# Kernel tuning notes

Hardware: AMD Instinct MI355X
Metric: run time of the kernel (lower is better)

Reference implementation:

```python
import jax, jax.numpy as jnp
import numpy as np

B, L, V, E_ENC, D_DEC, E_EMB = 256, 128, 4096, 1024, 1024, 512


def _lin(key, out_f, in_f, scale=0.02):
    k1, k2 = jax.random.split(key)
    return (jax.random.normal(k1, (out_f, in_f), jnp.float32) * scale,
            jax.random.normal(k2, (out_f,), jnp.float32) * scale)


def setup_inputs() -> dict:
    key = jax.random.key(0)
    ks = jax.random.split(key, 12)
    x = jax.random.normal(ks[0], (B, 1, V), jnp.float32)
    hidden = jax.random.normal(ks[1], (1, B, D_DEC), jnp.float32)
    enc_output = jax.random.normal(ks[2], (B, L, E_ENC), jnp.float32)
    W1_w, W1_b = _lin(ks[3], D_DEC, E_ENC)
    W2_w, W2_b = _lin(ks[4], D_DEC, D_DEC)
    V_w, V_b = _lin(ks[5], 1, D_DEC)
    out2emb_w, out2emb_b = _lin(ks[6], E_EMB, V)
    gru_wi, gru_bi = _lin(ks[7], 3 * D_DEC, E_EMB + E_ENC)
    gru_wh, gru_bh = _lin(ks[8], 3 * D_DEC, D_DEC)
    fc1_w, fc1_b = _lin(ks[9], E_EMB, D_DEC)
    fc2_w, fc2_b = _lin(ks[10], V, E_EMB)
    return dict(x=x, hidden=hidden, enc_output=enc_output,
                W1_w=W1_w, W1_b=W1_b, W2_w=W2_w, W2_b=W2_b, V_w=V_w, V_b=V_b,
                out2emb_w=out2emb_w, out2emb_b=out2emb_b,
                gru_wi=gru_wi, gru_wh=gru_wh, gru_bi=gru_bi, gru_bh=gru_bh,
                fc1_w=fc1_w, fc1_b=fc1_b, fc2_w=fc2_w, fc2_b=fc2_b)


def reference(x, hidden, enc_output, W1_w, W1_b, W2_w, W2_b, V_w, V_b,
              out2emb_w, out2emb_b, gru_wi, gru_wh, gru_bi, gru_bh,
              fc1_w, fc1_b, fc2_w, fc2_b):
    # --- Bahdanau additive attention ---
    h_t = hidden[-1][:, None, :]                                   # (B,1,dec)
    score = jnp.tanh(enc_output @ W1_w.T + W1_b + h_t @ W2_w.T + W2_b)  # (B,L,dec)
    attn = jax.nn.softmax(score @ V_w.T + V_b, axis=1)             # (B,L,1)
    context = jnp.sum(attn * enc_output, axis=1)                   # (B,enc)
    # --- embed previous output distribution ---
    x_emb = x @ out2emb_w.T + out2emb_b                            # (B,1,emb)
    rnn_in = jnp.concatenate([context[:, None, :], x_emb], -1)[:, 0, :]  # (B,emb+enc)
    # --- single GRU step (PyTorch gate layout r,z,n) ---
    h0 = hidden[0]
    gi = rnn_in @ gru_wi.T + gru_bi
    gh = h0 @ gru_wh.T + gru_bh
    ir, iz, inn = jnp.split(gi, 3, axis=-1)
    hr, hz, hn = jnp.split(gh, 3, axis=-1)
    r = jax.nn.sigmoid(ir + hr)
    z = jax.nn.sigmoid(iz + hz)
    n = jnp.tanh(inn + r * hn)
    h_new = (1.0 - z) * n + z * h0                                 # (B,dec)
    # --- output MLP ---
    out = jnp.tanh(h_new @ fc1_w.T + fc1_b) @ fc2_w.T + fc2_b      # (B,vocab)
    return out, h_new[None], attn
```

## Files before the change

### kernel.cpp

```cpp
#include <hip/hip_runtime.h>
#include <math.h>


#define B_   256
#define L_   128
#define V_   4096
#define ENC_ 1024
#define DEC_ 1024
#define EMB_ 512
#define MB_  1048576ull

typedef __bf16 bf16;
typedef __bf16 bf16x8 __attribute__((ext_vector_type(8)));
typedef __bf16 bf16x4 __attribute__((ext_vector_type(4)));
typedef float  f32x4  __attribute__((ext_vector_type(4)));

__device__ __forceinline__ float fast_tanh(float x) {
  float e = __builtin_amdgcn_exp2f(x * 2.88539008177792681472f);
  return 1.0f - 2.0f * __builtin_amdgcn_rcpf(e + 1.0f);
}
__device__ __forceinline__ float fast_sigmoid(float x) {
  return __builtin_amdgcn_rcpf(1.0f + __builtin_amdgcn_exp2f(-1.44269504088896f * x));
}

__device__ __forceinline__ void cp16(const void* g, void* l) {
  __builtin_amdgcn_global_load_lds(
      (const __attribute__((address_space(1))) void*)g,
      (__attribute__((address_space(3))) void*)l,
      16, 0, 0);
}

__device__ __forceinline__ bf16x8 ld8f(const float* f) {
  f32x4 a = *(const f32x4*)f;
  f32x4 b = *(const f32x4*)(f + 4);
  bf16x8 r;
  r[0] = (bf16)a[0]; r[1] = (bf16)a[1]; r[2] = (bf16)a[2]; r[3] = (bf16)a[3];
  r[4] = (bf16)b[0]; r[5] = (bf16)b[1]; r[6] = (bf16)b[2]; r[7] = (bf16)b[3];
  return r;
}


__device__ __forceinline__ void gemm64_f32(
    const float* __restrict__ A, const float* __restrict__ Brow,
    int strideA, int strideB, int kbeg, int kend, int row0,
    bf16* As, bf16* Bs, f32x4 acc[4])
{
  const int t   = threadIdx.x;
  const int lane = t & 63, w = t >> 6, q = lane >> 4, c16 = lane & 15;
  const int sr  = t >> 3, lb = t & 7;

  for (int k0 = kbeg; k0 < kend; k0 += 64) {
    bf16x8 va[2], vb[2];
#pragma unroll
    for (int ch = 0; ch < 2; ch++) {
      int r    = ch * 32 + sr;
      int gcol = k0 + ((lb ^ (r & 7)) << 3);
      va[ch] = ld8f(A    + (size_t)(row0 + r) * strideA + gcol);
      vb[ch] = ld8f(Brow + (size_t)r * strideB + gcol);
    }
#pragma unroll
    for (int ch = 0; ch < 2; ch++) {
      *(bf16x8*)&As[ch * 2048 + t * 8] = va[ch];
      *(bf16x8*)&Bs[ch * 2048 + t * 8] = vb[ch];
    }
    __syncthreads();
#pragma unroll
    for (int kkb = 0; kkb < 8; kkb += 4) {
      int rb = w * 16 + c16;
      bf16x8 bfr = *(const bf16x8*)&Bs[rb * 64 + (((kkb + q) ^ (rb & 7)) << 3)];
#pragma unroll
      for (int i = 0; i < 4; i++) {
        int ra = i * 16 + c16;
        bf16x8 af = *(const bf16x8*)&As[ra * 64 + (((kkb + q) ^ (ra & 7)) << 3)];
        acc[i] = __builtin_amdgcn_mfma_f32_16x16x32_bf16(af, bfr, acc[i], 0, 0, 0);
      }
    }
    __syncthreads();
  }
}

__global__ __launch_bounds__(256) void setup_k(
    const float* __restrict__ hidden, const float* __restrict__ W2,
    const float* __restrict__ wh, const float* __restrict__ W1_b,
    const float* __restrict__ W2_b, const float* __restrict__ gbh,
    const float* __restrict__ x, const float* __restrict__ o2e,
    const float* __restrict__ enc, const float* __restrict__ W1,
    const float* __restrict__ wi, const float* __restrict__ fc1w,
    const float* __restrict__ fc2w,
    bf16* __restrict__ enc_bf, bf16* __restrict__ W1_bf,
    bf16* __restrict__ wi_bf, bf16* __restrict__ fc1_bf,
    bf16* __restrict__ fc2_bf,
    bf16* __restrict__ u, bf16* __restrict__ gh, float* __restrict__ xe4)
{
  __shared__ __align__(16) bf16 As[64 * 64];
  __shared__ __align__(16) bf16 Bs[64 * 64];

  const int bid = blockIdx.x;
  const int t   = threadIdx.x;

  if (bid >= 384) {
    int i = bid - 384;
    const float* src; bf16* dst; int blk;
    if      (i < 8192) { src = enc;  dst = enc_bf; blk = i; }
    else if (i < 8448) { src = W1;   dst = W1_bf;  blk = i - 8192; }
    else if (i < 9600) { src = wi;   dst = wi_bf;  blk = i - 8448; }
    else if (i < 9728) { src = fc1w; dst = fc1_bf; blk = i - 9600; }
    else               { src = fc2w; dst = fc2_bf; blk = i - 9728; }
    const size_t base = (size_t)blk * 4096 + t * 16;
    const float* s = src + base;
    bf16* d = dst + base;
    *(bf16x8*)(d)     = ld8f(s);
    *(bf16x8*)(d + 8) = ld8f(s + 8);
    return;
  }

  const int lane = t & 63, w = t >> 6, q = lane >> 4, c16 = lane & 15;
  f32x4 acc[4] = {};

  if (bid < 256) {
    const int row0 = (bid >> 6) * 64;
    const int col0 = (bid & 63) * 64;
    const bool isU = (col0 < 1024);
    const float* Brow = isU ? (W2 + (size_t)col0 * 1024)
                            : (wh + (size_t)(col0 - 1024) * 1024);
    gemm64_f32(hidden, Brow, 1024, 1024, 0, 1024, row0, As, Bs, acc);

    const int gc = col0 + w * 16 + c16;
    float bias = isU ? (W1_b[gc] + W2_b[gc]) : gbh[gc - 1024];
#pragma unroll
    for (int i = 0; i < 4; i++) {
      int gr0 = row0 + i * 16 + q * 4;
#pragma unroll
      for (int r = 0; r < 4; r++) {
        float v = acc[i][r] + bias;
        if (isU) u[(size_t)(gr0 + r) * 1024 + gc] = (bf16)v;
        else     gh[(size_t)(gr0 + r) * 3072 + (gc - 1024)] = (bf16)v;
      }
    }
  } else {
    const int i3   = bid - 256;
    const int col0 = (i3 & 7) * 64;
    const int row0 = ((i3 >> 3) & 3) * 64;
    const int z    = i3 >> 5;
    gemm64_f32(x, o2e + (size_t)col0 * 4096, 4096, 4096,
               z * 1024, z * 1024 + 1024, row0, As, Bs, acc);

    const int gc = col0 + w * 16 + c16;
    float* out = xe4 + (size_t)z * 131072;
#pragma unroll
    for (int i = 0; i < 4; i++) {
      int gr0 = row0 + i * 16 + q * 4;
#pragma unroll
      for (int r = 0; r < 4; r++)
        out[(size_t)(gr0 + r) * 512 + gc] = acc[i][r];
    }
  }
}

__global__ __launch_bounds__(256) void score_f2(
    const bf16* __restrict__ A,
    const bf16* __restrict__ Bw,
    const bf16* __restrict__ u,
    const float* __restrict__ Vw,
    float* __restrict__ e_part)
{
  __shared__ __align__(16) bf16 As[128 * 64];
  __shared__ __align__(16) bf16 Bs[128 * 64];
  __shared__ float s_part[2][128];

  const int t    = threadIdx.x;
  const int lane = t & 63;
  const int w    = t >> 6;
  const int wm   = w >> 1;
  const int wn   = w & 1;
  const int q    = lane >> 4;
  const int c16  = lane & 15;
  const int sr   = t >> 3;
  const int lb   = t & 7;

  const int row0 = blockIdx.y * 128;
  const int b    = blockIdx.y;

  float rowsum[4][4] = {};

#pragma unroll 1
  for (int cbp = 0; cbp < 2; cbp++) {
    const int col0 = (blockIdx.x * 2 + cbp) * 128;
    f32x4 acc[4][4] = {};

    for (int k0 = 0; k0 < 1024; k0 += 64) {
#pragma unroll
      for (int ch = 0; ch < 4; ch++) {
        int r    = ch * 32 + sr;
        int gcol = k0 + ((lb ^ (r & 7)) << 3);
        cp16(A  + (size_t)(row0 + r) * 1024 + gcol, &As[ch * 2048 + t * 8]);
        cp16(Bw + (size_t)(col0 + r) * 1024 + gcol, &Bs[ch * 2048 + t * 8]);
      }
      __syncthreads();
#pragma unroll
      for (int kkb = 0; kkb < 8; kkb += 4) {
        bf16x8 af[4], bfr[4];
#pragma unroll
        for (int i = 0; i < 4; i++) {
          int ra = wm * 64 + i * 16 + c16;
          af[i] = *(const bf16x8*)&As[ra * 64 + (((kkb + q) ^ (ra & 7)) << 3)];
        }
#pragma unroll
        for (int j = 0; j < 4; j++) {
          int rb = wn * 64 + j * 16 + c16;
          bfr[j] = *(const bf16x8*)&Bs[rb * 64 + (((kkb + q) ^ (rb & 7)) << 3)];
        }
#pragma unroll
        for (int i = 0; i < 4; i++)
#pragma unroll
          for (int j = 0; j < 4; j++)
            acc[i][j] = __builtin_amdgcn_mfma_f32_16x16x32_bf16(af[i], bfr[j], acc[i][j], 0, 0, 0);
      }
      __syncthreads();
    }

#pragma unroll
    for (int i = 0; i < 4; i++) {
#pragma unroll
      for (int j = 0; j < 4; j++) {
        int gc   = col0 + wn * 64 + j * 16 + c16;
        float uc = (float)u[b * 1024 + gc];
        float vw = Vw[gc];
#pragma unroll
        for (int r = 0; r < 4; r++)
          rowsum[i][r] += fast_tanh(acc[i][j][r] + uc) * vw;
      }
    }
  }

#pragma unroll
  for (int i = 0; i < 4; i++) {
#pragma unroll
    for (int r = 0; r < 4; r++) {
      float v = rowsum[i][r];
      v += __shfl_xor(v, 1);
      v += __shfl_xor(v, 2);
      v += __shfl_xor(v, 4);
      v += __shfl_xor(v, 8);
      if (c16 == 0) s_part[wn][wm * 64 + i * 16 + q * 4 + r] = v;
    }
  }
  __syncthreads();
  if (t < 128)
    e_part[(size_t)blockIdx.x * 32768 + row0 + t] = s_part[0][t] + s_part[1][t];
}

__global__ __launch_bounds__(256) void softmax_f(
    const float* __restrict__ e_part,
    const bf16* __restrict__ enc,
    const float* __restrict__ xe4,
    const float* __restrict__ o2eb,
    float* __restrict__ attn_out,
    bf16* __restrict__ rnn_in)
{
  const int b = blockIdx.x;
  const int t = threadIdx.x;
  __shared__ float se[128];

  if (t < 128) {
    float s = 0.0f;
#pragma unroll
    for (int cb = 0; cb < 4; cb++) s += e_part[(size_t)cb * 32768 + b * 128 + t];
    se[t] = s;
  }
  __syncthreads();

  float m = -1e30f;
  for (int l = 0; l < 128; l++) m = fmaxf(m, se[l]);
  float sum = 0.0f;
  for (int l = 0; l < 128; l++) sum += expf(se[l] - m);
  float inv = 1.0f / sum;
  __syncthreads();
  if (t < 128) {
    float p = expf(se[t] - m) * inv;
    attn_out[b * 128 + t] = p;
    se[t] = p;
  }
  __syncthreads();

  float a0 = 0, a1 = 0, a2 = 0, a3 = 0;
  const bf16* ep = enc + (size_t)b * L_ * ENC_ + t * 4;
  for (int l = 0; l < 128; l++) {
    float p = se[l];
    bf16x4 v = *(const bf16x4*)(ep + (size_t)l * ENC_);
    a0 += p * (float)v[0]; a1 += p * (float)v[1];
    a2 += p * (float)v[2]; a3 += p * (float)v[3];
  }
  bf16x4 o;
  o[0] = (bf16)a0; o[1] = (bf16)a1; o[2] = (bf16)a2; o[3] = (bf16)a3;
  *(bf16x4*)(rnn_in + (size_t)b * 1536 + t * 4) = o;

#pragma unroll
  for (int jj = 0; jj < 2; jj++) {
    int j = jj * 256 + t;
    float v = o2eb[j];
#pragma unroll
    for (int z = 0; z < 4; z++) v += xe4[(size_t)z * 131072 + b * 512 + j];
    rnn_in[(size_t)b * 1536 + 1024 + j] = (bf16)v;
  }
}

template <int ACT, int OUTF32>
__global__ __launch_bounds__(256) void gemm_f(
    const bf16* __restrict__ A, const bf16* __restrict__ Bw,
    const float* __restrict__ bias1,
    void* __restrict__ C, int K, int out_ld)
{
  __shared__ __align__(16) bf16 As[64 * 64];
  __shared__ __align__(16) bf16 Bs[64 * 64];

  const int t    = threadIdx.x;
  const int lane = t & 63;
  const int w    = t >> 6;
  const int q    = lane >> 4;
  const int c16  = lane & 15;
  const int sr   = t >> 3;
  const int lb   = t & 7;
  const int row0 = blockIdx.y * 64;
  const int col0 = blockIdx.x * 64;

  f32x4 acc[4] = {};

  for (int k0 = 0; k0 < K; k0 += 64) {
#pragma unroll
    for (int ch = 0; ch < 2; ch++) {
      int r    = ch * 32 + sr;
      int gcol = k0 + ((lb ^ (r & 7)) << 3);
      cp16(A  + (size_t)(row0 + r) * K + gcol, &As[ch * 2048 + t * 8]);
      cp16(Bw + (size_t)(col0 + r) * K + gcol, &Bs[ch * 2048 + t * 8]);
    }
    __syncthreads();
#pragma unroll
    for (int kkb = 0; kkb < 8; kkb += 4) {
      int rb = w * 16 + c16;
      bf16x8 bfr = *(const bf16x8*)&Bs[rb * 64 + (((kkb + q) ^ (rb & 7)) << 3)];
#pragma unroll
      for (int i = 0; i < 4; i++) {
        int ra = i * 16 + c16;
        bf16x8 af = *(const bf16x8*)&As[ra * 64 + (((kkb + q) ^ (ra & 7)) << 3)];
        acc[i] = __builtin_amdgcn_mfma_f32_16x16x32_bf16(af, bfr, acc[i], 0, 0, 0);
      }
    }
    __syncthreads();
  }

  const int gc = col0 + w * 16 + c16;
  float bias = bias1[gc];
#pragma unroll
  for (int i = 0; i < 4; i++) {
    int gr0 = row0 + i * 16 + q * 4;
#pragma unroll
    for (int r = 0; r < 4; r++) {
      float v = acc[i][r] + bias;
      if (ACT == 1) v = fast_tanh(v);
      size_t off = (size_t)(gr0 + r) * out_ld + gc;
      if (OUTF32) ((float*)C)[off] = v;
      else        ((bf16*)C)[off] = (bf16)v;
    }
  }
}

__global__ __launch_bounds__(256) void gru_f(
    const bf16* __restrict__ gi, const bf16* __restrict__ gh,
    const float* __restrict__ h0,
    float* __restrict__ hnew_out, bf16* __restrict__ hnew_i)
{
  int idx = blockIdx.x * 256 + threadIdx.x;
  int b = idx >> 10, d = idx & 1023;
  const bf16* gib = gi + b * 3072;
  const bf16* ghb = gh + b * 3072;
  float ir = (float)gib[d], iz = (float)gib[1024 + d], in = (float)gib[2048 + d];
  float hr = (float)ghb[d], hz = (float)ghb[1024 + d], hn = (float)ghb[2048 + d];
  float r = fast_sigmoid(ir + hr);
  float z = fast_sigmoid(iz + hz);
  float n = fast_tanh(in + r * hn);
  float h = (1.0f - z) * n + z * h0[idx];
  hnew_out[idx] = h;
  hnew_i[idx]   = (bf16)h;
}

extern "C" void kernel_launch(void* const* d_in, const int* in_sizes, int n_in,
                              void* d_out, int out_size, void* d_ws, size_t ws_size,
                              hipStream_t stream) {
  const float* x      = (const float*)d_in[0];
  const float* hidden = (const float*)d_in[1];
  const float* enc    = (const float*)d_in[2];
  const float* W1_w   = (const float*)d_in[3];
  const float* W1_b   = (const float*)d_in[4];
  const float* W2_w   = (const float*)d_in[5];
  const float* W2_b   = (const float*)d_in[6];
  const float* V_w    = (const float*)d_in[7];
  const float* o2e_w  = (const float*)d_in[9];
  const float* o2e_b  = (const float*)d_in[10];
  const float* gru_wi = (const float*)d_in[11];
  const float* gru_wh = (const float*)d_in[12];
  const float* gru_bi = (const float*)d_in[13];
  const float* gru_bh = (const float*)d_in[14];
  const float* fc1_w  = (const float*)d_in[15];
  const float* fc1_b  = (const float*)d_in[16];
  const float* fc2_w  = (const float*)d_in[17];
  const float* fc2_b  = (const float*)d_in[18];

  float* out_main = (float*)d_out;
  float* out_h    = out_main + (size_t)B_ * V_;
  float* out_attn = out_h + (size_t)B_ * DEC_;

  char* ws = (char*)d_ws;
  bf16*  enc_bf  = (bf16*)(ws);
  bf16*  W1_bf   = (bf16*)(ws + 64 * MB_);
  bf16*  wi_bf   = (bf16*)(ws + 66 * MB_);
  bf16*  fc1_bf  = (bf16*)(ws + 75 * MB_);
  bf16*  fc2_bf  = (bf16*)(ws + 76 * MB_);
  bf16*  u_bf    = (bf16*)(ws + 80 * MB_);
  bf16*  gh_bf   = (bf16*)(ws + 80 * MB_ + 524288);
  float* e_part  = (float*)(ws + 82 * MB_);
  bf16*  gi_bf   = (bf16*)(ws + 82 * MB_ + 524288);
  bf16*  rnn_in  = (bf16*)(ws + 84 * MB_);
  bf16*  tbuf    = (bf16*)(ws + 84 * MB_ + 786432);
  bf16*  hnew_bf = (bf16*)(ws + 85 * MB_);
  float* xe4     = (float*)(ws + 85 * MB_ + 524288);

  setup_k<<<10624, 256, 0, stream>>>(
      hidden, W2_w, gru_wh, W1_b, W2_b, gru_bh, x, o2e_w,
      enc, W1_w, gru_wi, fc1_w, fc2_w,
      enc_bf, W1_bf, wi_bf, fc1_bf, fc2_bf, u_bf, gh_bf, xe4);

  score_f2<<<dim3(4, 256), 256, 0, stream>>>(enc_bf, W1_bf, u_bf, V_w, e_part);

  softmax_f<<<B_, 256, 0, stream>>>(e_part, enc_bf, xe4, o2e_b, out_attn, rnn_in);

  gemm_f<0, 0><<<dim3(48, 4), 256, 0, stream>>>(rnn_in, wi_bf, gru_bi, gi_bf, 1536, 3072);

  gru_f<<<(B_ * DEC_) / 256, 256, 0, stream>>>(gi_bf, gh_bf, hidden, out_h, hnew_bf);

  gemm_f<1, 0><<<dim3(8, 4), 256, 0, stream>>>(hnew_bf, fc1_bf, fc1_b, tbuf, 1024, 512);

  gemm_f<0, 1><<<dim3(64, 4), 256, 0, stream>>>(tbuf, fc2_bf, fc2_b, out_main, 512, 4096);
}
```

Baseline: 432.7 us.

## Rewrite attention score GEMM with 256x256 tiles and double-buffered LDS pipeline

The score kernel moves from 128x128 tiles with single-buffered LDS and a barrier-bound loop to 256x256 tiles on 512-thread blocks with two LDS stages. The next k-tile is prefetched while MFMAs run, and the blocks get a swizzled order for better L2 locality. The tanh and V-dot epilogue now runs once per tile instead of across two column passes, cutting global load traffic per FLOP. In exchange it uses much more LDS (128KB) and more accumulator registers per thread, which may limit occupancy.

```diff
diff --git a/kernel.cpp b/kernel.cpp
--- a/kernel.cpp
+++ b/kernel.cpp
@@ -157,97 +157,113 @@
   }
 }
 
-__global__ __launch_bounds__(256) void score_f2(
+__device__ __forceinline__ void stage_tile256(
+    const bf16* __restrict__ A, const bf16* __restrict__ Bw,
+    bf16* As, bf16* Bs, int row0, int col0, int k0, int t)
+{
+  const int sr = t >> 3, lb = t & 7;
+#pragma unroll
+  for (int ch = 0; ch < 4; ch++) {
+    int r    = ch * 64 + sr;
+    int gcol = k0 + ((lb ^ (r & 7)) << 3);
+    cp16(A  + (size_t)(row0 + r) * 1024 + gcol, &As[r * 64 + lb * 8]);
+    cp16(Bw + (size_t)(col0 + r) * 1024 + gcol, &Bs[r * 64 + lb * 8]);
+  }
+}
+
+__global__ __launch_bounds__(512, 2) void score_8p(
     const bf16* __restrict__ A,
     const bf16* __restrict__ Bw,
     const bf16* __restrict__ u,
     const float* __restrict__ Vw,
     float* __restrict__ e_part)
 {
-  __shared__ __align__(16) bf16 As[128 * 64];
-  __shared__ __align__(16) bf16 Bs[128 * 64];
-  __shared__ float s_part[2][128];
-
-  const int t    = threadIdx.x;
-  const int lane = t & 63;
-  const int w    = t >> 6;
-  const int wm   = w >> 1;
-  const int wn   = w & 1;
-  const int q    = lane >> 4;
-  const int c16  = lane & 15;
-  const int sr   = t >> 3;
-  const int lb   = t & 7;
-
-  const int row0 = blockIdx.y * 128;
-  const int b    = blockIdx.y;
-
-  float rowsum[4][4] = {};
-
-#pragma unroll 1
-  for (int cbp = 0; cbp < 2; cbp++) {
-    const int col0 = (blockIdx.x * 2 + cbp) * 128;
-    f32x4 acc[4][4] = {};
-
-    for (int k0 = 0; k0 < 1024; k0 += 64) {
-#pragma unroll
-      for (int ch = 0; ch < 4; ch++) {
-        int r    = ch * 32 + sr;
-        int gcol = k0 + ((lb ^ (r & 7)) << 3);
-        cp16(A  + (size_t)(row0 + r) * 1024 + gcol, &As[ch * 2048 + t * 8]);
-        cp16(Bw + (size_t)(col0 + r) * 1024 + gcol, &Bs[ch * 2048 + t * 8]);
-      }
-      __syncthreads();
-#pragma unroll
-      for (int kkb = 0; kkb < 8; kkb += 4) {
-        bf16x8 af[4], bfr[4];
-#pragma unroll
-        for (int i = 0; i < 4; i++) {
-          int ra = wm * 64 + i * 16 + c16;
-          af[i] = *(const bf16x8*)&As[ra * 64 + (((kkb + q) ^ (ra & 7)) << 3)];
-        }
-#pragma unroll
-        for (int j = 0; j < 4; j++) {
-          int rb = wn * 64 + j * 16 + c16;
-          bfr[j] = *(const bf16x8*)&Bs[rb * 64 + (((kkb + q) ^ (rb & 7)) << 3)];
-        }
-#pragma unroll
-        for (int i = 0; i < 4; i++)
-#pragma unroll
-          for (int j = 0; j < 4; j++)
-            acc[i][j] = __builtin_amdgcn_mfma_f32_16x16x32_bf16(af[i], bfr[j], acc[i][j], 0, 0, 0);
-      }
-      __syncthreads();
-    }
-
-#pragma unroll
-    for (int i = 0; i < 4; i++) {
-#pragma unroll
-      for (int j = 0; j < 4; j++) {
-        int gc   = col0 + wn * 64 + j * 16 + c16;
-        float uc = (float)u[b * 1024 + gc];
-        float vw = Vw[gc];
-#pragma unroll
-        for (int r = 0; r < 4; r++)
-          rowsum[i][r] += fast_tanh(acc[i][j][r] + uc) * vw;
-      }
-    }
-  }
-
-#pragma unroll
-  for (int i = 0; i < 4; i++) {
+  __shared__ __align__(16) bf16 sA[2 * 16384];
+  __shared__ __align__(16) bf16 sB[2 * 16384];
+  __shared__ float s_part[4][256];
+
+  const int t = threadIdx.x;
+  const int wg  = blockIdx.x;
+  const int swz = (wg & 7) * 64 + (wg >> 3);
+  const int bx  = swz & 3;
+  const int by  = swz >> 2;
+  const int row0 = by * 256;
+  const int col0 = bx * 256;
+
+  const int lane = t & 63, w = t >> 6;
+  const int wm = w >> 2, wn = w & 3;
+  const int q = lane >> 4, c16 = lane & 15;
+
+  stage_tile256(A, Bw, sA, sB, row0, col0, 0, t);
+  stage_tile256(A, Bw, sA + 16384, sB + 16384, row0, col0, 64, t);
+  asm volatile("s_waitcnt vmcnt(8)" ::: "memory");
+  __builtin_amdgcn_s_barrier();
+
+  f32x4 acc[8][4] = {};
+
+  for (int kt = 0; kt < 16; ++kt) {
+    const bf16* As = sA + (kt & 1) * 16384;
+    const bf16* Bs = sB + (kt & 1) * 16384;
+
+    bf16x8 bfr[2][4];
+#pragma unroll
+    for (int j = 0; j < 4; j++) {
+      const int rb = wn * 64 + j * 16 + c16;
+      bfr[0][j] = *(const bf16x8*)&Bs[rb * 64 + (((0 + q) ^ (rb & 7)) << 3)];
+      bfr[1][j] = *(const bf16x8*)&Bs[rb * 64 + (((4 + q) ^ (rb & 7)) << 3)];
+    }
+    __builtin_amdgcn_s_setprio(1);
+#pragma unroll
+    for (int i = 0; i < 8; i++) {
+      const int ra = wm * 128 + i * 16 + c16;
+      bf16x8 a0 = *(const bf16x8*)&As[ra * 64 + (((0 + q) ^ (ra & 7)) << 3)];
+      bf16x8 a1 = *(const bf16x8*)&As[ra * 64 + (((4 + q) ^ (ra & 7)) << 3)];
+#pragma unroll
+      for (int j = 0; j < 4; j++)
+        acc[i][j] = __builtin_amdgcn_mfma_f32_16x16x32_bf16(a0, bfr[0][j], acc[i][j], 0, 0, 0);
+#pragma unroll
+      for (int j = 0; j < 4; j++)
+        acc[i][j] = __builtin_amdgcn_mfma_f32_16x16x32_bf16(a1, bfr[1][j], acc[i][j], 0, 0, 0);
+    }
+    __builtin_amdgcn_s_setprio(0);
+    __builtin_amdgcn_s_barrier();
+    if (kt < 14) {
+      stage_tile256(A, Bw, sA + (kt & 1) * 16384, sB + (kt & 1) * 16384,
+                    row0, col0, (kt + 2) * 64, t);
+      asm volatile("s_waitcnt vmcnt(8)" ::: "memory");
+    } else {
+      asm volatile("s_waitcnt vmcnt(0)" ::: "memory");
+    }
+    __builtin_amdgcn_s_barrier();
+  }
+
+  const int b = by * 2 + wm;
+  float uc[4], vw[4];
+#pragma unroll
+  for (int j = 0; j < 4; j++) {
+    const int gc = col0 + wn * 64 + j * 16 + c16;
+    uc[j] = (float)u[b * 1024 + gc];
+    vw[j] = Vw[gc];
+  }
+#pragma unroll
+  for (int i = 0; i < 8; i++) {
 #pragma unroll
     for (int r = 0; r < 4; r++) {
-      float v = rowsum[i][r];
+      float v = 0.0f;
+#pragma unroll
+      for (int j = 0; j < 4; j++)
+        v += fast_tanh(acc[i][j][r] + uc[j]) * vw[j];
       v += __shfl_xor(v, 1);
       v += __shfl_xor(v, 2);
       v += __shfl_xor(v, 4);
       v += __shfl_xor(v, 8);
-      if (c16 == 0) s_part[wn][wm * 64 + i * 16 + q * 4 + r] = v;
+      if (c16 == 0) s_part[wn][wm * 128 + i * 16 + q * 4 + r] = v;
     }
   }
   __syncthreads();
-  if (t < 128)
-    e_part[(size_t)blockIdx.x * 32768 + row0 + t] = s_part[0][t] + s_part[1][t];
+  if (t < 256)
+    e_part[(size_t)bx * 32768 + row0 + t] =
+        s_part[0][t] + s_part[1][t] + s_part[2][t] + s_part[3][t];
 }
 
 __global__ __launch_bounds__(256) void softmax_f(
@@ -430,7 +446,7 @@
       enc, W1_w, gru_wi, fc1_w, fc2_w,
       enc_bf, W1_bf, wi_bf, fc1_bf, fc2_bf, u_bf, gh_bf, xe4);
 
-  score_f2<<<dim3(4, 256), 256, 0, stream>>>(enc_bf, W1_bf, u_bf, V_w, e_part);
+  score_8p<<<512, 512, 0, stream>>>(enc_bf, W1_bf, u_bf, V_w, e_part);
 
   softmax_f<<<B_, 256, 0, stream>>>(e_part, enc_bf, xe4, o2e_b, out_attn, rnn_in);
 
```

Result: faster. 416.4 us (-3.7%).
